# Optimization experiments

Measured on AMD Instinct MI355X. Metric: run time of the kernel, lower is better.

Reference implementation:

```python
import jax, jax.numpy as jnp
import numpy as np

B, N, C, W = 256, 4096, 16, 10
L = N - W + 1
EPS = 1e-5


def setup_inputs() -> dict:
    key = jax.random.key(0)
    ks = jax.random.split(key, 6)
    def lin(k, shape, fan_in):
        # mimic nn.Linear default init scale ~ U(-1/sqrt(fan), 1/sqrt(fan))
        b = 1.0 / np.sqrt(fan_in)
        return jax.random.uniform(k, shape, jnp.float32, -b, b)
    return {
        "x": jax.random.normal(ks[0], (B, N, C, 2), jnp.float32),
        "W_in_real": lin(ks[1], (C, L), L),      # per-channel input filter (real)
        "W_in_imag": lin(ks[2], (C, L), L),      # per-channel input filter (imag)
        "W_nl": lin(ks[3], (C, 2, 2 * C), 2 * C),  # per-channel Linear(2C -> 2)
        "W_out_real": lin(ks[4], (C, W), W),      # per-channel output filter (real)
        "W_out_imag": lin(ks[5], (C, W), W),      # per-channel output filter (imag)
        "gamma": jnp.ones((C,), jnp.float32),     # BatchNorm1d weight
        "beta": jnp.zeros((C,), jnp.float32),     # BatchNorm1d bias
    }


def _depthwise_valid(x_bcn, w_cl):
    # sliding dot-products f[:, c, id] = sum_l x[:, c, id+l] * w[c, l]
    # == depthwise 1D valid correlation: [B,C,N] * [C,L] -> [B,C,W]
    nC = w_cl.shape[0]
    return jax.lax.conv_general_dilated(
        x_bcn, w_cl[:, None, :], window_strides=(1,), padding='VALID',
        dimension_numbers=('NCH', 'OIH', 'NCH'), feature_group_count=nC)


def reference(x, W_in_real, W_in_imag, W_nl, W_out_real, W_out_imag, gamma, beta):
    xr = jnp.transpose(x[..., 0], (0, 2, 1))  # [B,C,N]
    xi = jnp.transpose(x[..., 1], (0, 2, 1))
    # stage 1: per-channel windowed filters + amplitude (|f|^2) scaling
    fr = jnp.transpose(_depthwise_valid(xr, W_in_real), (0, 2, 1))  # [B,W,C]
    fi = jnp.transpose(_depthwise_valid(xi, W_in_imag), (0, 2, 1))  # [B,W,C]
    amp = fr * fr + fi * fi
    fr = amp * fr
    fi = amp * fi
    # stage 2: per-channel nonlin Linear(2C -> 2) on cat([real, imag])
    tf = jnp.concatenate([fr, fi], axis=-1)            # [B,W,2C]
    nl = jnp.einsum('bwi,coi->bwco', tf, W_nl)         # [B,W,C,2]
    nr, ni = nl[..., 0], nl[..., 1]                    # [B,W,C]
    # stage 3: per-channel output filters over the out_window dim
    out_r = jnp.einsum('bwc,cw->bc', nr, W_out_real)   # [B,C]
    out_i = jnp.einsum('bwc,cw->bc', ni, W_out_imag)   # [B,C]
    out = jnp.stack([out_r, out_i], axis=-1)           # [B,C,2]
    # BatchNorm1d(n_channels) in training mode: stats over (batch, last) per channel
    mean = out.mean(axis=(0, 2), keepdims=True)
    var = out.var(axis=(0, 2), keepdims=True)
    return (out - mean) / jnp.sqrt(var + EPS) * gamma[None, :, None] + beta[None, :, None]
```

## Files before the change

### kernel.cpp

```cpp
#include <hip/hip_runtime.h>

#define BB 256
#define NN 4096
#define CC 16
#define WW 10
#define LL 4087
#define EPSF 1e-5f

__global__ __launch_bounds__(256) void pack_weights(const float* __restrict__ Wr,
                                                    const float* __restrict__ Wi,
                                                    float2* __restrict__ pk) {
    int tg = blockIdx.x * 256 + threadIdx.x;
    int n = tg >> 4, c = tg & 15;
    float2 v = make_float2(0.f, 0.f);
    if (n < LL) { v.x = Wr[c * LL + n]; v.y = Wi[c * LL + n]; }
    pk[tg] = v;
}

template <bool PK>
__global__ __launch_bounds__(1024, 4) void fused_main(const float* __restrict__ x,
                                                      const float2* __restrict__ pk,
                                                      const float* __restrict__ Wr,
                                                      const float* __restrict__ Wi,
                                                      const float* __restrict__ Wnl,
                                                      const float* __restrict__ Wor,
                                                      const float* __restrict__ Woi,
                                                      float* __restrict__ outraw) {
    const int b = blockIdx.x;
    const int tid = threadIdx.x;
    const int tc = tid >> 4;
    const int c = tid & 15;
    const int n0 = tc * 64;

    const float2* __restrict__ x2 = (const float2*)x + (size_t)b * (NN * CC) + (n0 * 16 + c);
    const float2* __restrict__ pkp = pk + (n0 * 16 + c);

    float tr[9], ti[9];
    float fr[WW], fi[WW];
#pragma unroll
    for (int w = 0; w < WW; ++w) { fr[w] = 0.f; fi[w] = 0.f; }

#pragma unroll
    for (int j = 0; j < 9; ++j) {
        const int m = n0 - 9 + j;
        float vr = 0.f, vi = 0.f;
        if (PK) {
            if (m >= 0) { const float2 t = pk[m * 16 + c]; vr = t.x; vi = t.y; }
        } else {
            const int mc = m < 0 ? 0 : m;
            const float a = Wr[c * LL + mc], q = Wi[c * LL + mc];
            vr = (m >= 0) ? a : 0.f;
            vi = (m >= 0) ? q : 0.f;
        }
        tr[j] = vr;
        ti[j] = vi;
    }

#pragma unroll 1
    for (int g = 0; g < 4; ++g) {
        const int nb = n0 + g * 16;
        float2 xb[16], wb[16];
#pragma unroll
        for (int p = 0; p < 16; ++p) {
            xb[p] = x2[p * 16];
            if (PK) {
                wb[p] = pkp[p * 16];
            } else {
                const int n = nb + p;
                const int nc2 = (n < LL) ? n : (LL - 1);
                const float a = Wr[c * LL + nc2], q = Wi[c * LL + nc2];
                wb[p].x = (n < LL) ? a : 0.f;
                wb[p].y = (n < LL) ? q : 0.f;
            }
        }
        x2 += 256;
        pkp += 256;

#pragma unroll
        for (int p = 0; p < 16; ++p) {
#pragma unroll
            for (int w = 0; w < WW; ++w) {
                const int q = p - w;
                const float wr_ = (q >= 0) ? wb[q].x : tr[q + 9];
                const float wi_ = (q >= 0) ? wb[q].y : ti[q + 9];
                fr[w] += xb[p].x * wr_;
                fi[w] += xb[p].y * wi_;
            }
        }
#pragma unroll
        for (int j = 0; j < 9; ++j) { tr[j] = wb[j + 7].x; ti[j] = wb[j + 7].y; }
    }

#pragma unroll
    for (int w = 0; w < WW; ++w) {
        fr[w] += __shfl_xor(fr[w], 16);
        fr[w] += __shfl_xor(fr[w], 32);
        fi[w] += __shfl_xor(fi[w], 16);
        fi[w] += __shfl_xor(fi[w], 32);
    }
    __shared__ float red[16][320];
    __shared__ float F2[320];
    __shared__ float nls[320];
    const int lane = tid & 63, wave = tid >> 6;
    if (lane < 16) {
#pragma unroll
        for (int w = 0; w < WW; ++w) {
            red[wave][lane * 20 + w] = fr[w];
            red[wave][lane * 20 + 10 + w] = fi[w];
        }
    }
    __syncthreads();
    if (tid < 320) {
        float s = 0.f;
#pragma unroll
        for (int k = 0; k < 16; ++k) s += red[k][tid];
        F2[tid] = s;
    }
    __syncthreads();
    if (tid < 160) {
        const int cc = tid / 10, w = tid % 10;
        const float a = F2[cc * 20 + w], q = F2[cc * 20 + 10 + w];
        const float amp = a * a + q * q;
        F2[cc * 20 + w] = a * amp;
        F2[cc * 20 + 10 + w] = q * amp;
    }
    __syncthreads();
    if (tid < 320) {
        const int cc = tid / 20, rem = tid % 20, o = rem / 10, w = rem % 10;
        const float* __restrict__ wn = Wnl + (cc * 2 + o) * 32;
        float acc = 0.f;
#pragma unroll
        for (int i = 0; i < 16; ++i) acc += F2[i * 20 + w] * wn[i];
#pragma unroll
        for (int i = 0; i < 16; ++i) acc += F2[i * 20 + 10 + w] * wn[16 + i];
        nls[tid] = acc;
    }
    __syncthreads();
    if (tid < 32) {
        const int cc = tid >> 1, o = tid & 1;
        const float* __restrict__ wo = (o == 0 ? Wor : Woi) + cc * WW;
        float acc = 0.f;
#pragma unroll
        for (int w = 0; w < WW; ++w) acc += nls[cc * 20 + o * 10 + w] * wo[w];
        outraw[b * 32 + cc * 2 + o] = acc;
    }
}

__global__ __launch_bounds__(256) void bnorm(float* __restrict__ out,
                                             const float* __restrict__ gamma,
                                             const float* __restrict__ beta) {
    const int c = blockIdx.x;
    const int t = threadIdx.x;
    const float v0 = out[t * 32 + c * 2 + 0];
    const float v1 = out[t * 32 + c * 2 + 1];
    float s = v0 + v1;
    float ss = v0 * v0 + v1 * v1;
#pragma unroll
    for (int off = 32; off > 0; off >>= 1) {
        s += __shfl_down(s, off, 64);
        ss += __shfl_down(ss, off, 64);
    }
    __shared__ float ls[8];
    const int wave = t >> 6, lane = t & 63;
    if (lane == 0) { ls[wave * 2] = s; ls[wave * 2 + 1] = ss; }
    __syncthreads();
    const float S = ls[0] + ls[2] + ls[4] + ls[6];
    const float SS = ls[1] + ls[3] + ls[5] + ls[7];
    const float mean = S * (1.f / 512.f);
    const float var = SS * (1.f / 512.f) - mean * mean;
    const float scale = gamma[c] * rsqrtf(var + EPSF);
    const float sh = beta[c];
    out[t * 32 + c * 2 + 0] = (v0 - mean) * scale + sh;
    out[t * 32 + c * 2 + 1] = (v1 - mean) * scale + sh;
}

extern "C" void kernel_launch(void* const* d_in, const int* in_sizes, int n_in,
                              void* d_out, int out_size, void* d_ws, size_t ws_size,
                              hipStream_t stream) {
    const float* x     = (const float*)d_in[0];
    const float* Wr    = (const float*)d_in[1];
    const float* Wi    = (const float*)d_in[2];
    const float* Wnl   = (const float*)d_in[3];
    const float* Wor   = (const float*)d_in[4];
    const float* Woi   = (const float*)d_in[5];
    const float* gamma = (const float*)d_in[6];
    const float* beta  = (const float*)d_in[7];
    float* out = (float*)d_out;

    const size_t pk_bytes = (size_t)NN * CC * sizeof(float2);
    float2* pk = (float2*)d_ws;
    const bool use_pk = (ws_size >= pk_bytes);

    if (use_pk) {
        hipLaunchKernelGGL(pack_weights, dim3(256), dim3(256), 0, stream, Wr, Wi, pk);
        hipLaunchKernelGGL((fused_main<true>), dim3(BB), dim3(1024), 0, stream,
                           x, pk, Wr, Wi, Wnl, Wor, Woi, out);
    } else {
        hipLaunchKernelGGL((fused_main<false>), dim3(BB), dim3(1024), 0, stream,
                           x, pk, Wr, Wi, Wnl, Wor, Woi, out);
    }
    hipLaunchKernelGGL(bnorm, dim3(CC), dim3(256), 0, stream, out, gamma, beta);
}
```

Measured before the change: 211.0 us.

## Stage x and packed weights through double-buffered LDS via global_load_lds

Replaces the register-streaming main kernel with one that copies 32 KB tiles of x and packed weights straight into LDS using the global_load_lds builtin, double-buffered so the next tile's load overlaps compute on the current one. Each thread then reads 4 positions plus a 13-wide weight halo from LDS, so overlapping weight reuse comes from shared memory rather than per-thread global loads. It uses about 132 KB of LDS per 1024-thread block and adds a barrier per tile, which limits residency to one block per CU and risks exceeding the LDS limit.

```diff
diff --git a/kernel.cpp b/kernel.cpp
--- a/kernel.cpp
+++ b/kernel.cpp
@@ -6,6 +6,10 @@
 #define WW 10
 #define LL 4087
 #define EPSF 1e-5f
+
+#define GLOAD16(gsrc, ldst)                                                                  \
+    __builtin_amdgcn_global_load_lds((const __attribute__((address_space(1))) void*)(gsrc),  \
+                                     (__attribute__((address_space(3))) void*)(ldst), 16, 0, 0)
 
 __global__ __launch_bounds__(256) void pack_weights(const float* __restrict__ Wr,
                                                     const float* __restrict__ Wi,
@@ -17,15 +21,160 @@
     pk[tg] = v;
 }
 
-template <bool PK>
-__global__ __launch_bounds__(1024, 4) void fused_main(const float* __restrict__ x,
-                                                      const float2* __restrict__ pk,
-                                                      const float* __restrict__ Wr,
-                                                      const float* __restrict__ Wi,
-                                                      const float* __restrict__ Wnl,
-                                                      const float* __restrict__ Wor,
-                                                      const float* __restrict__ Woi,
-                                                      float* __restrict__ outraw) {
+__global__ __launch_bounds__(1024, 4) void fused_lds(const float* __restrict__ x,
+                                                     const float2* __restrict__ pk,
+                                                     const float* __restrict__ Wnl,
+                                                     const float* __restrict__ Wor,
+                                                     const float* __restrict__ Woi,
+                                                     float* __restrict__ outraw) {
+    __shared__ __align__(16) char smem[135168];
+
+    const int b = blockIdx.x;
+    const int tid = threadIdx.x;
+    const int c = tid & 15;
+    const int tc = tid >> 4;
+    const int base = tc * 4;
+    const int lane = tid & 63, wave = tid >> 6;
+    const int l16 = lane * 16;
+
+    const char* __restrict__ xsrc = (const char*)x + (size_t)b * (NN * CC * 8);
+    const char* __restrict__ psrc = (const char*)pk;
+
+    float fr[WW], fi[WW];
+#pragma unroll
+    for (int w = 0; w < WW; ++w) { fr[w] = 0.f; fi[w] = 0.f; }
+
+    {
+#pragma unroll
+        for (int k = 0; k < 2; ++k) {
+            const int i = wave * 2 + k;
+            GLOAD16(xsrc + i * 1024 + l16, smem + i * 1024);
+            GLOAD16(psrc + i * 1024 + l16, smem + 65536 + i * 1024);
+        }
+        if (wave < 2) {
+            const int i = 32 + wave;
+            GLOAD16(psrc + i * 1024 + l16, smem + 65536 + i * 1024);
+        }
+    }
+    __syncthreads();
+
+#pragma unroll 1
+    for (int t = 0; t < 16; ++t) {
+        if (t < 15) {
+            const int t1 = t + 1, pb_ = t1 & 1;
+            const char* xs = xsrc + (size_t)t1 * 32768;
+            char* xd = smem + pb_ * 32768;
+#pragma unroll
+            for (int k = 0; k < 2; ++k) {
+                const int i = wave * 2 + k;
+                GLOAD16(xs + i * 1024 + l16, xd + i * 1024);
+            }
+            const char* ps = psrc + (size_t)(t1 * 256 - 16) * 128;
+            char* pd = smem + 65536 + pb_ * 34816;
+#pragma unroll
+            for (int k = 0; k < 2; ++k) {
+                const int i = wave * 2 + k;
+                GLOAD16(ps + i * 1024 + l16, pd + i * 1024);
+            }
+            if (wave < 2) {
+                const int i = 32 + wave;
+                GLOAD16(ps + i * 1024 + l16, pd + i * 1024);
+            }
+        }
+
+        const float2* __restrict__ xb = (const float2*)(smem + (t & 1) * 32768);
+        const float2* __restrict__ pb = (const float2*)(smem + 65536 + (t & 1) * 34816);
+
+        float2 wv[13];
+        if (t == 0) {
+#pragma unroll
+            for (int k = 0; k < 13; ++k) {
+                const int slot = base + k - 9;
+                const int sc = slot < 0 ? 0 : slot;
+                const float2 tmp = pb[sc * 16 + c];
+                wv[k].x = (slot >= 0) ? tmp.x : 0.f;
+                wv[k].y = (slot >= 0) ? tmp.y : 0.f;
+            }
+        } else {
+#pragma unroll
+            for (int k = 0; k < 13; ++k) wv[k] = pb[(base + 7 + k) * 16 + c];
+        }
+        float2 xv[4];
+#pragma unroll
+        for (int j = 0; j < 4; ++j) xv[j] = xb[(base + j) * 16 + c];
+#pragma unroll
+        for (int j = 0; j < 4; ++j) {
+#pragma unroll
+            for (int w = 0; w < WW; ++w) {
+                const int k = j - w + 9;
+                fr[w] += xv[j].x * wv[k].x;
+                fi[w] += xv[j].y * wv[k].y;
+            }
+        }
+        __syncthreads();
+    }
+
+#pragma unroll
+    for (int w = 0; w < WW; ++w) {
+        fr[w] += __shfl_xor(fr[w], 16);
+        fr[w] += __shfl_xor(fr[w], 32);
+        fi[w] += __shfl_xor(fi[w], 16);
+        fi[w] += __shfl_xor(fi[w], 32);
+    }
+    float (*red)[320] = (float (*)[320])smem;
+    float* F2 = (float*)(smem + 20480);
+    float* nls = (float*)(smem + 21760);
+    if (lane < 16) {
+#pragma unroll
+        for (int w = 0; w < WW; ++w) {
+            red[wave][lane * 20 + w] = fr[w];
+            red[wave][lane * 20 + 10 + w] = fi[w];
+        }
+    }
+    __syncthreads();
+    if (tid < 320) {
+        float s = 0.f;
+#pragma unroll
+        for (int k = 0; k < 16; ++k) s += red[k][tid];
+        F2[tid] = s;
+    }
+    __syncthreads();
+    if (tid < 160) {
+        const int cc = tid / 10, w = tid % 10;
+        const float a = F2[cc * 20 + w], q = F2[cc * 20 + 10 + w];
+        const float amp = a * a + q * q;
+        F2[cc * 20 + w] = a * amp;
+        F2[cc * 20 + 10 + w] = q * amp;
+    }
+    __syncthreads();
+    if (tid < 320) {
+        const int cc = tid / 20, rem = tid % 20, o = rem / 10, w = rem % 10;
+        const float* __restrict__ wn = Wnl + (cc * 2 + o) * 32;
+        float acc = 0.f;
+#pragma unroll
+        for (int i = 0; i < 16; ++i) acc += F2[i * 20 + w] * wn[i];
+#pragma unroll
+        for (int i = 0; i < 16; ++i) acc += F2[i * 20 + 10 + w] * wn[16 + i];
+        nls[tid] = acc;
+    }
+    __syncthreads();
+    if (tid < 32) {
+        const int cc = tid >> 1, o = tid & 1;
+        const float* __restrict__ wo = (o == 0 ? Wor : Woi) + cc * WW;
+        float acc = 0.f;
+#pragma unroll
+        for (int w = 0; w < WW; ++w) acc += nls[cc * 20 + o * 10 + w] * wo[w];
+        outraw[b * 32 + cc * 2 + o] = acc;
+    }
+}
+
+__global__ __launch_bounds__(1024, 4) void fused_main_nopk(const float* __restrict__ x,
+                                                           const float* __restrict__ Wr,
+                                                           const float* __restrict__ Wi,
+                                                           const float* __restrict__ Wnl,
+                                                           const float* __restrict__ Wor,
+                                                           const float* __restrict__ Woi,
+                                                           float* __restrict__ outraw) {
     const int b = blockIdx.x;
     const int tid = threadIdx.x;
     const int tc = tid >> 4;
@@ -33,7 +182,6 @@
     const int n0 = tc * 64;
 
     const float2* __restrict__ x2 = (const float2*)x + (size_t)b * (NN * CC) + (n0 * 16 + c);
-    const float2* __restrict__ pkp = pk + (n0 * 16 + c);
 
     float tr[9], ti[9];
     float fr[WW], fi[WW];
@@ -43,17 +191,10 @@
 #pragma unroll
     for (int j = 0; j < 9; ++j) {
         const int m = n0 - 9 + j;
-        float vr = 0.f, vi = 0.f;
-        if (PK) {
-            if (m >= 0) { const float2 t = pk[m * 16 + c]; vr = t.x; vi = t.y; }
-        } else {
-            const int mc = m < 0 ? 0 : m;
-            const float a = Wr[c * LL + mc], q = Wi[c * LL + mc];
-            vr = (m >= 0) ? a : 0.f;
-            vi = (m >= 0) ? q : 0.f;
-        }
-        tr[j] = vr;
-        ti[j] = vi;
+        const int mc = m < 0 ? 0 : m;
+        const float a = Wr[c * LL + mc], q = Wi[c * LL + mc];
+        tr[j] = (m >= 0) ? a : 0.f;
+        ti[j] = (m >= 0) ? q : 0.f;
     }
 
 #pragma unroll 1
@@ -63,19 +204,13 @@
 #pragma unroll
         for (int p = 0; p < 16; ++p) {
             xb[p] = x2[p * 16];
-            if (PK) {
-                wb[p] = pkp[p * 16];
-            } else {
-                const int n = nb + p;
-                const int nc2 = (n < LL) ? n : (LL - 1);
-                const float a = Wr[c * LL + nc2], q = Wi[c * LL + nc2];
-                wb[p].x = (n < LL) ? a : 0.f;
-                wb[p].y = (n < LL) ? q : 0.f;
-            }
+            const int n = nb + p;
+            const int nc2 = (n < LL) ? n : (LL - 1);
+            const float a = Wr[c * LL + nc2], q = Wi[c * LL + nc2];
+            wb[p].x = (n < LL) ? a : 0.f;
+            wb[p].y = (n < LL) ? q : 0.f;
         }
         x2 += 256;
-        pkp += 256;
-
 #pragma unroll
         for (int p = 0; p < 16; ++p) {
 #pragma unroll
@@ -193,11 +328,11 @@
 
     if (use_pk) {
         hipLaunchKernelGGL(pack_weights, dim3(256), dim3(256), 0, stream, Wr, Wi, pk);
-        hipLaunchKernelGGL((fused_main<true>), dim3(BB), dim3(1024), 0, stream,
-                           x, pk, Wr, Wi, Wnl, Wor, Woi, out);
+        hipLaunchKernelGGL(fused_lds, dim3(BB), dim3(1024), 0, stream,
+                           x, pk, Wnl, Wor, Woi, out);
     } else {
-        hipLaunchKernelGGL((fused_main<false>), dim3(BB), dim3(1024), 0, stream,
-                           x, pk, Wr, Wi, Wnl, Wor, Woi, out);
+        hipLaunchKernelGGL(fused_main_nopk, dim3(BB), dim3(1024), 0, stream,
+                           x, Wr, Wi, Wnl, Wor, Woi, out);
     }
     hipLaunchKernelGGL(bnorm, dim3(CC), dim3(256), 0, stream, out, gamma, beta);
 }
```

New measurement: 212.2 us. Within noise of the previous version (+0.6%).
